# Optimization experiments

Measured on AMD Instinct MI355X. Metric: run time of the kernel, lower is better.

## Reference

```python
import jax, jax.numpy as jnp
import numpy as np

N_NODES = 100000


def gcn_conv(x, W, b, src, dst, n_nodes):
    """PyG GCNConv: symmetric-normalized scatter-add with self loops.
    src/dst already include self loops. x: [N, Fin], W: [Fin, Fout], b: [Fout]."""
    xw = x @ W  # [N, Fout]
    ones = jnp.ones(dst.shape[0], dtype=x.dtype)
    deg = jax.ops.segment_sum(ones, dst, num_segments=n_nodes)  # [N]
    dinv = jnp.where(deg > 0, jax.lax.rsqrt(deg), 0.0)
    norm = dinv[src] * dinv[dst]  # [E]
    msg = xw[src] * norm[:, None]  # [E, Fout]
    out = jax.ops.segment_sum(msg, dst, num_segments=n_nodes)  # [N, Fout]
    return out + b


def setup_inputs() -> dict:
    key = jax.random.key(0)
    k1, k2, k3, k4, k5 = jax.random.split(key, 5)
    in_ch, hid = 64, 64
    x = jax.random.normal(k1, (N_NODES, in_ch), dtype=jnp.float32)
    edge_index = jax.random.randint(k2, (2, 1200000), 0, N_NODES, dtype=jnp.int64)
    # Glorot-ish init for GCN linear layers (bias=True by PyG default)
    W1 = jax.random.normal(k3, (in_ch, hid), dtype=jnp.float32) / np.sqrt(in_ch)
    b1 = jnp.zeros((hid,), dtype=jnp.float32)
    W2 = jax.random.normal(k4, (hid, hid), dtype=jnp.float32) / np.sqrt(hid)
    b2 = jnp.zeros((hid,), dtype=jnp.float32)
    return {"x": x, "edge_index": edge_index, "W1": W1, "b1": b1, "W2": W2, "b2": b2}


def reference(x, edge_index, W1, b1, W2, b2):
    n = x.shape[0]
    loop = jnp.arange(n, dtype=edge_index.dtype)
    src = jnp.concatenate([edge_index[0], loop])  # add self loops
    dst = jnp.concatenate([edge_index[1], loop])
    h = jax.nn.relu(gcn_conv(x, W1, b1, src, dst, n))
    out = gcn_conv(h, W2, b2, src, dst, n)
    return out
```

## Files before the change

### kernel.cpp

```cpp
#include <hip/hip_runtime.h>
#include <hip/hip_fp16.h>

#define FDIM 64
#define SEG 512
#define SEG_SHIFT 9
#define NSEGMAX 256
#define SCAP 8192
#define GSTRIDE 8
#define PB_EDGES 8192

__global__ void detect_dtype_kernel(const int* ei, int nsamp, int* flag, int* gcount, int glen) {
    __shared__ int any_nz;
    if (threadIdx.x == 0) any_nz = 0;
    __syncthreads();
    int local = 0;
    for (int i = threadIdx.x; i < nsamp; i += blockDim.x) {
        if (ei[2 * i + 1] != 0) local = 1;
    }
    if (local) atomicOr(&any_nz, 1);
    for (int i = threadIdx.x; i < glen; i += blockDim.x) gcount[i] = 0;
    __syncthreads();
    if (threadIdx.x == 0) flag[0] = (any_nz == 0) ? 1 : 0;
}

__global__ __launch_bounds__(256) void bucket_place(const void* ei, const int* flag, int E,
                                                    int nseg,
                                                    int* __restrict__ gcount,
                                                    int2* __restrict__ parts) {
    __shared__ int lhist[NSEGMAX];
    __shared__ int lbase[NSEGMAX];
    __shared__ int loff[NSEGMAX];
    int is64 = flag[0];
    int t = threadIdx.x;
    const long long* q64 = (const long long*)ei;
    const int* q32 = (const int*)ei;
    int base = blockIdx.x * PB_EDGES;
    for (int i = t; i < nseg; i += 256) { lhist[i] = 0; loff[i] = 0; }
    __syncthreads();
    #pragma unroll 4
    for (int u = 0; u < PB_EDGES / 256; u++) {
        int i = base + u * 256 + t;
        if (i < E) {
            int d = is64 ? (int)q64[E + i] : q32[E + i];
            atomicAdd(&lhist[d >> SEG_SHIFT], 1);
        }
    }
    __syncthreads();
    for (int i = t; i < nseg; i += 256)
        lbase[i] = (lhist[i] > 0) ? atomicAdd(&gcount[i * GSTRIDE], lhist[i]) : 0;
    __syncthreads();
    #pragma unroll 4
    for (int u = 0; u < PB_EDGES / 256; u++) {
        int i = base + u * 256 + t;
        if (i < E) {
            int s, d;
            if (is64) { s = (int)q64[i]; d = (int)q64[E + i]; }
            else      { s = q32[i];      d = q32[E + i]; }
            int bk = d >> SEG_SHIFT;
            int off = atomicAdd(&loff[bk], 1);
            int pos = lbase[bk] + off;
            if (pos < SCAP) parts[(size_t)bk * SCAP + pos] = make_int2(s, d);
        }
    }
}

__global__ __launch_bounds__(256) void place_sort(const int2* __restrict__ parts,
                                                  const int* __restrict__ gcount,
                                                  int* __restrict__ csr,
                                                  int* __restrict__ rowstart,
                                                  int* __restrict__ degv,
                                                  float* __restrict__ dinv, int N) {
    __shared__ int hist[SEG];
    __shared__ int cur[SEG];
    __shared__ int A[256], B[256];
    int s = blockIdx.x;
    int t = threadIdx.x;
    int nbase = s << SEG_SHIFT;
    hist[t] = 0; hist[t + 256] = 0;
    __syncthreads();
    int cnt = gcount[s * GSTRIDE]; if (cnt > SCAP) cnt = SCAP;
    const int2* pg = parts + (size_t)s * SCAP;
    for (int j = t; j < cnt; j += 256) atomicAdd(&hist[pg[j].y & (SEG - 1)], 1);
    __syncthreads();
    int p = hist[2 * t] + hist[2 * t + 1];
    A[t] = p; __syncthreads();
    int* in = A; int* out = B;
    for (int off = 1; off < 256; off <<= 1) {
        out[t] = in[t] + ((t >= off) ? in[t - off] : 0);
        __syncthreads();
        int* z = in; in = out; out = z;
    }
    int esc = (t == 0) ? 0 : in[t - 1];
    cur[2 * t] = esc;
    cur[2 * t + 1] = esc + hist[2 * t];
    __syncthreads();
    for (int i = t; i < SEG; i += 256) {
        int n = nbase + i;
        if (n < N) {
            rowstart[n] = s * SCAP + cur[i];
            degv[n] = hist[i];
            dinv[n] = rsqrtf((float)(hist[i] + 1));
        }
    }
    __syncthreads();
    for (int j = t; j < cnt; j += 256) {
        int2 e = pg[j];
        int r = e.y & (SEG - 1);
        int off = atomicAdd(&cur[r], 1);
        csr[(size_t)s * SCAP + off] = e.x;
    }
}

template <typename TIN>
__global__ __launch_bounds__(256, 4) void gemm_scale(const TIN* __restrict__ x,
                                                     const float* __restrict__ W,
                                                     const float* __restrict__ dinv,
                                                     __half* __restrict__ y16, int N) {
    __shared__ float Xl[64 * 68];
    __shared__ float Wl[64 * 64];
    int t = threadIdx.x;
    int nbase = blockIdx.x * 64;
    for (int i = t; i < 1024; i += 256) {
        ((float4*)Wl)[i] = ((const float4*)W)[i];
    }
    for (int i = t; i < 1024; i += 256) {
        int flat = i * 4;
        int n = flat >> 6, k = flat & 63;
        int g = nbase + n;
        float4 v;
        if (g < N) {
            if constexpr (sizeof(TIN) == 2) {
                const __half2* hp = (const __half2*)((const __half*)x + (size_t)g * FDIM + k);
                float2 a = __half22float2(hp[0]);
                float2 c = __half22float2(hp[1]);
                v = make_float4(a.x, a.y, c.x, c.y);
            } else {
                v = *(const float4*)((const float*)x + (size_t)g * FDIM + k);
            }
        } else {
            v = make_float4(0.f, 0.f, 0.f, 0.f);
        }
        *(float4*)&Xl[n * 68 + k] = v;
    }
    __syncthreads();

    int fr = t & 15;
    int ng = t >> 4;
    float acc[4][4] = {{0.f}};
    #pragma unroll 4
    for (int kc = 0; kc < 16; kc++) {
        float4 xa[4], wa[4];
        #pragma unroll
        for (int i = 0; i < 4; i++) xa[i] = *(float4*)&Xl[(ng * 4 + i) * 68 + kc * 4];
        #pragma unroll
        for (int j = 0; j < 4; j++) wa[j] = *(float4*)&Wl[(kc * 4 + j) * 64 + fr * 4];
        #pragma unroll
        for (int i = 0; i < 4; i++) {
            acc[i][0] += xa[i].x * wa[0].x + xa[i].y * wa[1].x + xa[i].z * wa[2].x + xa[i].w * wa[3].x;
            acc[i][1] += xa[i].x * wa[0].y + xa[i].y * wa[1].y + xa[i].z * wa[2].y + xa[i].w * wa[3].y;
            acc[i][2] += xa[i].x * wa[0].z + xa[i].y * wa[1].z + xa[i].z * wa[2].z + xa[i].w * wa[3].z;
            acc[i][3] += xa[i].x * wa[0].w + xa[i].y * wa[1].w + xa[i].z * wa[2].w + xa[i].w * wa[3].w;
        }
    }
    #pragma unroll
    for (int i = 0; i < 4; i++) {
        int g = nbase + ng * 4 + i;
        if (g < N) {
            float dv = dinv[g];
            __half2 ha = __floats2half2_rn(acc[i][0] * dv, acc[i][1] * dv);
            __half2 hb = __floats2half2_rn(acc[i][2] * dv, acc[i][3] * dv);
            union { __half2 h[2]; uint2 u; } cvt;
            cvt.h[0] = ha; cvt.h[1] = hb;
            *(uint2*)(y16 + (size_t)g * FDIM + fr * 4) = cvt.u;
        }
    }
}

__device__ __forceinline__ float4 half4_to_float4(uint2 u) {
    float2 a = __half22float2(*(__half2*)&u.x);
    float2 b = __half22float2(*(__half2*)&u.y);
    return make_float4(a.x, a.y, b.x, b.y);
}

template <bool RELU, typename OUT_T>
__global__ __launch_bounds__(256) void gather(const int* __restrict__ rowstart,
                                              const int* __restrict__ degv,
                                              const int* __restrict__ csr,
                                              const __half* __restrict__ y16,
                                              const float* __restrict__ dinv,
                                              const float* __restrict__ b,
                                              OUT_T* __restrict__ out, int N) {
    int lane = threadIdx.x & 63;
    int n = blockIdx.x * 4 + (threadIdx.x >> 6);
    if (n >= N) return;
    int q = lane >> 4;
    int fl = lane & 15;
    int start = rowstart[n];
    int end = start + degv[n];
    uint2 su = make_uint2(0u, 0u);
    if (q == 0) su = *(const uint2*)(y16 + (size_t)n * FDIM + 4 * fl);
    float ax = 0.f, ay = 0.f, az = 0.f, aw = 0.f;
    for (int base = start; base < end; base += 64) {
        int m = end - base; if (m > 64) m = 64;
        int idx = (lane < m) ? csr[base + lane] : 0;
        for (int j = 0; j < m; j += 16) {
            int e0 = j + q, e1 = j + 4 + q, e2 = j + 8 + q, e3 = j + 12 + q;
            int s0 = __shfl(idx, (e0 < m) ? e0 : (m - 1));
            int s1 = __shfl(idx, (e1 < m) ? e1 : (m - 1));
            int s2 = __shfl(idx, (e2 < m) ? e2 : (m - 1));
            int s3 = __shfl(idx, (e3 < m) ? e3 : (m - 1));
            uint2 u0 = *(const uint2*)(y16 + (size_t)s0 * FDIM + 4 * fl);
            uint2 u1 = *(const uint2*)(y16 + (size_t)s1 * FDIM + 4 * fl);
            uint2 u2 = *(const uint2*)(y16 + (size_t)s2 * FDIM + 4 * fl);
            uint2 u3 = *(const uint2*)(y16 + (size_t)s3 * FDIM + 4 * fl);
            if (e0 < m) { float4 f = half4_to_float4(u0); ax += f.x; ay += f.y; az += f.z; aw += f.w; }
            if (e1 < m) { float4 f = half4_to_float4(u1); ax += f.x; ay += f.y; az += f.z; aw += f.w; }
            if (e2 < m) { float4 f = half4_to_float4(u2); ax += f.x; ay += f.y; az += f.z; aw += f.w; }
            if (e3 < m) { float4 f = half4_to_float4(u3); ax += f.x; ay += f.y; az += f.z; aw += f.w; }
        }
    }
    ax += __shfl_xor(ax, 16); ay += __shfl_xor(ay, 16);
    az += __shfl_xor(az, 16); aw += __shfl_xor(aw, 16);
    ax += __shfl_xor(ax, 32); ay += __shfl_xor(ay, 32);
    az += __shfl_xor(az, 32); aw += __shfl_xor(aw, 32);
    if (q == 0) {
        float4 sf = half4_to_float4(su);
        float dv = dinv[n];
        float4 bb = ((const float4*)b)[fl];
        float ox = (ax + sf.x) * dv + bb.x;
        float oy = (ay + sf.y) * dv + bb.y;
        float oz = (az + sf.z) * dv + bb.z;
        float ow = (aw + sf.w) * dv + bb.w;
        if (RELU) {
            ox = fmaxf(ox, 0.f); oy = fmaxf(oy, 0.f);
            oz = fmaxf(oz, 0.f); ow = fmaxf(ow, 0.f);
        }
        if constexpr (sizeof(OUT_T) == 2) {
            union { __half2 h[2]; uint2 u; } cvt;
            cvt.h[0] = __floats2half2_rn(ox, oy);
            cvt.h[1] = __floats2half2_rn(oz, ow);
            *(uint2*)((__half*)out + (size_t)n * FDIM + 4 * fl) = cvt.u;
        } else {
            *(float4*)((float*)out + (size_t)n * FDIM + 4 * fl) = make_float4(ox, oy, oz, ow);
        }
    }
}

static inline size_t roundup256(size_t x) { return (x + 255) & ~(size_t)255; }

extern "C" void kernel_launch(void* const* d_in, const int* in_sizes, int n_in,
                              void* d_out, int out_size, void* d_ws, size_t ws_size,
                              hipStream_t stream) {
    const float* x  = (const float*)d_in[0];
    const void*  ei = d_in[1];
    const float* W1 = (const float*)d_in[2];
    const float* b1 = (const float*)d_in[3];
    const float* W2 = (const float*)d_in[4];
    const float* b2 = (const float*)d_in[5];
    float* out = (float*)d_out;

    int N = out_size / FDIM;
    int E = in_sizes[1] / 2;
    int nseg = (N + SEG - 1) >> SEG_SHIFT;
    if (nseg > NSEGMAX) nseg = NSEGMAX;
    int nblk_p = (E + PB_EDGES - 1) / PB_EDGES;

    char* p = (char*)d_ws;
    float* dinv    = (float*)p;  p += roundup256((size_t)N * 4);
    __half* y16    = (__half*)p; p += roundup256((size_t)N * FDIM * 2);
    __half* h16    = (__half*)p; p += roundup256((size_t)N * FDIM * 2);
    int* gcount    = (int*)p;    p += (size_t)NSEGMAX * GSTRIDE * 4;
    int* flag      = (int*)p;    p += 256;
    int* rowstart  = (int*)p;    p += roundup256((size_t)N * 4);
    int* degv      = (int*)p;    p += roundup256((size_t)N * 4);
    int* csr       = (int*)p;    p += (size_t)nseg * SCAP * 4;
    int2* parts    = (int2*)p;   p += (size_t)nseg * SCAP * sizeof(int2);

    detect_dtype_kernel<<<1, 256, 0, stream>>>((const int*)ei, 2048, flag,
                                               gcount, NSEGMAX * GSTRIDE);
    bucket_place<<<nblk_p, 256, 0, stream>>>(ei, flag, E, nseg, gcount, parts);
    place_sort<<<nseg, 256, 0, stream>>>(parts, gcount, csr, rowstart, degv, dinv, N);

    int gemm_grid = (N + 63) / 64;
    int gath_grid = (N + 3) / 4;

    gemm_scale<float><<<gemm_grid, 256, 0, stream>>>(x, W1, dinv, y16, N);
    gather<true, __half><<<gath_grid, 256, 0, stream>>>(rowstart, degv, csr, y16, dinv, b1, h16, N);

    gemm_scale<__half><<<gemm_grid, 256, 0, stream>>>(h16, W2, dinv, y16, N);
    gather<false, float><<<gath_grid, 256, 0, stream>>>(rowstart, degv, csr, y16, dinv, b2, out, N);
}
```

Baseline: 175.4 us.

## Use packed fp16 dot2 in dense transform and halve per-block edge count

The node-feature GEMM now stages X and W in shared memory as packed half2 pairs along K and accumulates with the v_dot2 fp32 builtin, halving LDS footprint and the number of multiply-add instructions. W is transposed into K-pair packing on load. The per-block edge count constant is also halved, which changes the grid for the bucketing stage. Rounding fp32 inputs to fp16 before the matmul reduces accuracy.

```diff
diff --git a/kernel.cpp b/kernel.cpp
--- a/kernel.cpp
+++ b/kernel.cpp
@@ -7,7 +7,9 @@
 #define NSEGMAX 256
 #define SCAP 8192
 #define GSTRIDE 8
-#define PB_EDGES 8192
+#define PB_EDGES 4096
+
+typedef _Float16 h2_t __attribute__((ext_vector_type(2)));
 
 __global__ void detect_dtype_kernel(const int* ei, int nsamp, int* flag, int* gcount, int glen) {
     __shared__ int any_nz;
@@ -116,50 +118,59 @@
                                                      const float* __restrict__ W,
                                                      const float* __restrict__ dinv,
                                                      __half* __restrict__ y16, int N) {
-    __shared__ float Xl[64 * 68];
-    __shared__ float Wl[64 * 64];
+    __shared__ h2_t Xl[64 * 34];
+    __shared__ h2_t Wl[32 * 64];
     int t = threadIdx.x;
     int nbase = blockIdx.x * 64;
-    for (int i = t; i < 1024; i += 256) {
-        ((float4*)Wl)[i] = ((const float4*)W)[i];
+    for (int i = t; i < 2048; i += 256) {
+        int k2 = i >> 6, f = i & 63;
+        float w0 = W[(2 * k2) * FDIM + f];
+        float w1 = W[(2 * k2 + 1) * FDIM + f];
+        h2_t pk; pk.x = (_Float16)w0; pk.y = (_Float16)w1;
+        Wl[i] = pk;
     }
     for (int i = t; i < 1024; i += 256) {
         int flat = i * 4;
         int n = flat >> 6, k = flat & 63;
         int g = nbase + n;
-        float4 v;
+        h2_t a, c;
         if (g < N) {
             if constexpr (sizeof(TIN) == 2) {
-                const __half2* hp = (const __half2*)((const __half*)x + (size_t)g * FDIM + k);
-                float2 a = __half22float2(hp[0]);
-                float2 c = __half22float2(hp[1]);
-                v = make_float4(a.x, a.y, c.x, c.y);
+                uint2 u = *(const uint2*)((const __half*)x + (size_t)g * FDIM + k);
+                a = *(h2_t*)&u.x; c = *(h2_t*)&u.y;
             } else {
-                v = *(const float4*)((const float*)x + (size_t)g * FDIM + k);
+                float4 v = *(const float4*)((const float*)x + (size_t)g * FDIM + k);
+                a.x = (_Float16)v.x; a.y = (_Float16)v.y;
+                c.x = (_Float16)v.z; c.y = (_Float16)v.w;
             }
         } else {
-            v = make_float4(0.f, 0.f, 0.f, 0.f);
-        }
-        *(float4*)&Xl[n * 68 + k] = v;
+            a.x = (_Float16)0.f; a.y = (_Float16)0.f; c = a;
+        }
+        Xl[n * 34 + (k >> 1)] = a;
+        Xl[n * 34 + (k >> 1) + 1] = c;
     }
     __syncthreads();
 
     int fr = t & 15;
     int ng = t >> 4;
     float acc[4][4] = {{0.f}};
-    #pragma unroll 4
-    for (int kc = 0; kc < 16; kc++) {
-        float4 xa[4], wa[4];
+    #pragma unroll 8
+    for (int k2 = 0; k2 < 32; k2++) {
+        h2_t xa[4], wa[4];
         #pragma unroll
-        for (int i = 0; i < 4; i++) xa[i] = *(float4*)&Xl[(ng * 4 + i) * 68 + kc * 4];
+        for (int i = 0; i < 4; i++) xa[i] = Xl[(ng * 4 + i) * 34 + k2];
         #pragma unroll
-        for (int j = 0; j < 4; j++) wa[j] = *(float4*)&Wl[(kc * 4 + j) * 64 + fr * 4];
+        for (int j = 0; j < 4; j++) wa[j] = Wl[k2 * 64 + fr * 4 + j];
         #pragma unroll
         for (int i = 0; i < 4; i++) {
-            acc[i][0] += xa[i].x * wa[0].x + xa[i].y * wa[1].x + xa[i].z * wa[2].x + xa[i].w * wa[3].x;
-            acc[i][1] += xa[i].x * wa[0].y + xa[i].y * wa[1].y + xa[i].z * wa[2].y + xa[i].w * wa[3].y;
-            acc[i][2] += xa[i].x * wa[0].z + xa[i].y * wa[1].z + xa[i].z * wa[2].z + xa[i].w * wa[3].z;
-            acc[i][3] += xa[i].x * wa[0].w + xa[i].y * wa[1].w + xa[i].z * wa[2].w + xa[i].w * wa[3].w;
+            #pragma unroll
+            for (int j = 0; j < 4; j++) {
+#if __has_builtin(__builtin_amdgcn_fdot2)
+                acc[i][j] = __builtin_amdgcn_fdot2(xa[i], wa[j], acc[i][j], false);
+#else
+                acc[i][j] += (float)xa[i].x * (float)wa[j].x + (float)xa[i].y * (float)wa[j].y;
+#endif
+            }
         }
     }
     #pragma unroll
```

Measured after the change: 156.1 us. 11.0% less time.
